# Kernel optimization log

Measured on AMD Instinct MI355X. Metric: run time of the kernel, lower is better.

The kernel has to match this reference:

```python
import jax, jax.numpy as jnp
import numpy as np

B, C_IN, C_OUT, C_KEY, N = 8, 512, 512, 256, 2048


def setup_inputs() -> dict:
    key = jax.random.key(0)
    k1, k2, k3, k4 = jax.random.split(key, 4)
    x = jax.random.normal(k1, (B, C_IN, N), dtype=jnp.float32)
    # Conv1d(kernel=1, bias=False) weights -> plain linear maps over channel dim
    Wq = jax.random.normal(k2, (C_KEY, C_IN), dtype=jnp.float32) * (1.0 / np.sqrt(C_IN))
    Wk = jax.random.normal(k3, (C_KEY, C_IN), dtype=jnp.float32) * (1.0 / np.sqrt(C_IN))
    Wv = jax.random.normal(k4, (C_OUT, C_IN), dtype=jnp.float32) * (1.0 / np.sqrt(C_IN))
    return {"x": x, "Wq": Wq, "Wk": Wk, "Wv": Wv}


def reference(x, Wq, Wk, Wv):
    # 1x1 conv projections: [B, C, N] -> [B, Ck/Co, N]
    q = jnp.einsum("oc,bcn->bon", Wq, x)
    k = jnp.einsum("oc,bcn->bon", Wk, x)
    v = jnpqv = jnp.einsum("oc,bcn->bon", Wv, x)
    # sim_map[b,i,j] = sum_c k[b,c,i] * q[b,c,j]  (unscaled)
    sim = jnp.einsum("bci,bcj->bij", k, q)  # [B, N, N]
    attn = jax.nn.softmax(sim, axis=-1)
    # out = value @ sim_map, then permute(0,2,1) -> [B, N, C_out]
    out = jnp.einsum("bck,bkm->bmc", jnpqv, attn)
    return out
```

## Files before the change

kernel.cpp:

```cpp
#include <hip/hip_runtime.h>

typedef _Float16 half8 __attribute__((ext_vector_type(8)));
typedef _Float16 half4v __attribute__((ext_vector_type(4)));
typedef _Float16 half2v __attribute__((ext_vector_type(2)));
typedef float f32x4 __attribute__((ext_vector_type(4)));

#define ASYNC_CP16(gp, lp)                                       \
  __builtin_amdgcn_global_load_lds(                              \
      (const __attribute__((address_space(1))) void*)(gp),       \
      (__attribute__((address_space(3))) void*)(lp), 16, 0, 0)

__global__ __launch_bounds__(256) void conv_w(const float* __restrict__ Wq,
                                              const float* __restrict__ Wk,
                                              const float* __restrict__ Wv,
                                              _Float16* __restrict__ Wb) {
  int idx = blockIdx.x * 256 + threadIdx.x;
  int row = idx >> 9;
  float v;
  if (row < 256)      v = Wq[idx];
  else if (row < 512) v = Wk[idx - 256 * 512];
  else                v = Wv[idx - 512 * 512];
  Wb[idx] = (_Float16)v;
}

__global__ __launch_bounds__(256) void conv_xT(const float* __restrict__ x,
                                               _Float16* __restrict__ xT) {
  __shared__ float T[32][33];
  const int b = blockIdx.z;
  const int n0 = blockIdx.x * 32, c0 = blockIdx.y * 32;
  const int t = threadIdx.x;
  const float* xb = x + (size_t)b * 512 * 2048;
  const int n2 = t & 15, cr = t >> 4;
#pragma unroll
  for (int r = 0; r < 2; r++) {
    int c = cr + r * 16;
    float2 v = *(const float2*)&xb[(size_t)(c0 + c) * 2048 + n0 + n2 * 2];
    T[c][n2 * 2] = v.x;
    T[c][n2 * 2 + 1] = v.y;
  }
  __syncthreads();
  _Float16* xtb = xT + (size_t)b * 2048 * 512;
  const int c2 = t & 15, nr = t >> 4;
#pragma unroll
  for (int r = 0; r < 2; r++) {
    int n = nr + r * 16;
    half2v h;
    h[0] = (_Float16)T[c2 * 2][n];
    h[1] = (_Float16)T[c2 * 2 + 1][n];
    *(half2v*)&xtb[(size_t)(n0 + n) * 512 + c0 + c2 * 2] = h;
  }
}

template <typename OutT, bool TR, bool STATS, bool PROJ3>
__global__ __launch_bounds__(256) void gemm_nt(
    const _Float16* __restrict__ A, const _Float16* __restrict__ B,
    OutT* __restrict__ C, OutT* __restrict__ C2, int K, int lda, int ldb,
    int ldc, int ldc2, long sA, long sB, long sC, float* __restrict__ pm,
    float* __restrict__ ps) {
  A += (size_t)blockIdx.z * sA;
  B += (size_t)blockIdx.z * sB;
  C += (size_t)blockIdx.z * sC;
  if constexpr (PROJ3) C2 += (size_t)blockIdx.z * sC;
  const int m_blk = blockIdx.y * 128, n_blk = blockIdx.x * 128;

  __shared__ _Float16 As[3][4096];
  __shared__ _Float16 Bs[3][4096];

  const int t = threadIdx.x;
  const int lane = t & 63, wave = t >> 6;
  const int quad = lane >> 4, l16 = lane & 15;
  const int wm = (wave & 1) * 64, wn = (wave >> 1) * 64;

  const int srow = 16 * wave + (lane >> 2);
  const int schunk = (lane & 3) ^ ((lane >> 3) & 3);
  const _Float16* gA0 = A + (size_t)(m_blk + srow) * lda + schunk * 8;
  const _Float16* gA1 = gA0 + (size_t)64 * lda;
  const _Float16* gB0 = B + (size_t)(n_blk + srow) * ldb + schunk * 8;
  const _Float16* gB1 = gB0 + (size_t)64 * ldb;
  const int lofs = wave * 512 + lane * 8;

  const int rchunk = (quad ^ ((l16 >> 1) & 3)) * 8;

  f32x4 acc[4][4] = {};

  ASYNC_CP16(gA0, &As[0][lofs]);
  ASYNC_CP16(gA1, &As[0][lofs + 2048]);
  ASYNC_CP16(gB0, &Bs[0][lofs]);
  ASYNC_CP16(gB1, &Bs[0][lofs + 2048]);
  if (32 < K) {
    ASYNC_CP16(gA0 + 32, &As[1][lofs]);
    ASYNC_CP16(gA1 + 32, &As[1][lofs + 2048]);
    ASYNC_CP16(gB0 + 32, &Bs[1][lofs]);
    ASYNC_CP16(gB1 + 32, &Bs[1][lofs + 2048]);
  }

  int ib = 0;
  for (int k0 = 0; k0 < K; k0 += 32) {
    if (k0 + 32 < K) {
      asm volatile("s_waitcnt vmcnt(4)\n\ts_barrier" ::: "memory");
    } else {
      asm volatile("s_waitcnt vmcnt(0)\n\ts_barrier" ::: "memory");
    }
    if (k0 + 64 < K) {
      int nb = ib + 2;
      if (nb >= 3) nb -= 3;
      ASYNC_CP16(gA0 + k0 + 64, &As[nb][lofs]);
      ASYNC_CP16(gA1 + k0 + 64, &As[nb][lofs + 2048]);
      ASYNC_CP16(gB0 + k0 + 64, &Bs[nb][lofs]);
      ASYNC_CP16(gB1 + k0 + 64, &Bs[nb][lofs + 2048]);
    }
    half8 af[4], bf[4];
#pragma unroll
    for (int i = 0; i < 4; i++) {
      af[i] = *(const half8*)&As[ib][(wm + i * 16 + l16) * 32 + rchunk];
      bf[i] = *(const half8*)&Bs[ib][(wn + i * 16 + l16) * 32 + rchunk];
    }
#pragma unroll
    for (int i = 0; i < 4; i++)
#pragma unroll
      for (int j = 0; j < 4; j++)
        acc[i][j] =
            __builtin_amdgcn_mfma_f32_16x16x32_f16(af[i], bf[j], acc[i][j], 0, 0, 0);
    ib++;
    if (ib == 3) ib = 0;
  }

#pragma unroll
  for (int i = 0; i < 4; i++) {
    const int m0 = m_blk + wm + i * 16 + quad * 4;
#pragma unroll
    for (int j = 0; j < 4; j++) {
      const int n0 = n_blk + wn + j * 16 + l16;
      if constexpr (PROJ3) {
        if (m_blk < 512) {
          half4v h;
#pragma unroll
          for (int r = 0; r < 4; r++) h[r] = (_Float16)acc[i][j][r];
          *(half4v*)&C[(size_t)n0 * ldc + m0] = h;
        } else {
#pragma unroll
          for (int r = 0; r < 4; r++)
            C2[(size_t)(m0 - 512 + r) * ldc2 + n0] = (OutT)acc[i][j][r];
        }
      } else if constexpr (TR) {
        if constexpr (sizeof(OutT) == 4) {
          *(f32x4*)&C[(size_t)n0 * ldc + m0] = acc[i][j];
        } else {
          half4v h;
#pragma unroll
          for (int r = 0; r < 4; r++) h[r] = (_Float16)acc[i][j][r];
          if constexpr (STATS) {
#pragma unroll
            for (int r = 0; r < 4; r++) acc[i][j][r] = (float)h[r];
          }
          *(half4v*)&C[(size_t)n0 * ldc + m0] = h;
        }
      } else {
#pragma unroll
        for (int r = 0; r < 4; r++)
          C[(size_t)(m0 + r) * ldc + n0] = (OutT)acc[i][j][r];
      }
    }
  }

  if constexpr (STATS) {
    __shared__ float sred[2][128][2];
    const int wng = wave >> 1;
    float bmax[4][4], bsum[4][4];
#pragma unroll
    for (int i = 0; i < 4; i++) {
#pragma unroll
      for (int r = 0; r < 4; r++) {
        float mx = acc[i][0][r];
#pragma unroll
        for (int j = 1; j < 4; j++) mx = fmaxf(mx, acc[i][j][r]);
#pragma unroll
        for (int d = 1; d < 16; d <<= 1)
          mx = fmaxf(mx, __shfl_xor(mx, d, 64));
        float es = 0.f;
#pragma unroll
        for (int j = 0; j < 4; j++) es += __expf(acc[i][j][r] - mx);
#pragma unroll
        for (int d = 1; d < 16; d <<= 1) es += __shfl_xor(es, d, 64);
        bmax[i][r] = mx;
        bsum[i][r] = es;
      }
    }
    if (l16 == 0) {
#pragma unroll
      for (int i = 0; i < 4; i++)
#pragma unroll
        for (int r = 0; r < 4; r++) {
          int ml = wm + i * 16 + quad * 4 + r;
          sred[wng][ml][0] = bmax[i][r];
          sred[wng][ml][1] = bsum[i][r];
        }
    }
    __syncthreads();
    if (t < 128) {
      float m0 = sred[0][t][0], s0 = sred[0][t][1];
      float m1 = sred[1][t][0], s1 = sred[1][t][1];
      float M = fmaxf(m0, m1);
      float S = s0 * __expf(m0 - M) + s1 * __expf(m1 - M);
      size_t o = ((size_t)blockIdx.z * 16 + blockIdx.x) * 2048 + m_blk + t;
      pm[o] = M;
      ps[o] = S;
    }
  }
}

__global__ __launch_bounds__(256) void colstats2(const float* __restrict__ pm,
                                                 const float* __restrict__ ps,
                                                 float* __restrict__ shift) {
  const int idx = blockIdx.x * 256 + threadIdx.x;
  const int b = idx >> 11, col = idx & 2047;
  const float* pmb = pm + (size_t)b * 16 * 2048 + col;
  const float* psb = ps + (size_t)b * 16 * 2048 + col;
  float m = -3.0e38f;
#pragma unroll
  for (int i = 0; i < 16; i++) m = fmaxf(m, pmb[(size_t)i * 2048]);
  float s = 0.f;
#pragma unroll
  for (int i = 0; i < 16; i++)
    s += psb[(size_t)i * 2048] * __expf(pmb[(size_t)i * 2048] - m);
  shift[idx] = m + __logf(s);
}

__global__ __launch_bounds__(256) void attnscale(_Float16* __restrict__ simH,
                                                 const float* __restrict__ shift) {
  const size_t b = blockIdx.y;
  const size_t g = (size_t)blockIdx.x * 256 + threadIdx.x;
  const int col = (int)(g & 255) * 8;
  _Float16* p = simH + b * (2048ull * 2048) + g * 8;
  half8 h = *(const half8*)p;
  f32x4 s0 = *(const f32x4*)(shift + b * 2048 + col);
  f32x4 s1 = *(const f32x4*)(shift + b * 2048 + col + 4);
  half8 o;
#pragma unroll
  for (int i = 0; i < 4; i++) {
    o[i] = (_Float16)__expf((float)h[i] - s0[i]);
    o[i + 4] = (_Float16)__expf((float)h[i + 4] - s1[i]);
  }
  *(half8*)p = o;
}

extern "C" void kernel_launch(void* const* d_in, const int* in_sizes, int n_in,
                              void* d_out, int out_size, void* d_ws,
                              size_t ws_size, hipStream_t stream) {
  const float* x = (const float*)d_in[0];
  const float* Wq = (const float*)d_in[1];
  const float* Wk = (const float*)d_in[2];
  const float* Wv = (const float*)d_in[3];
  float* out = (float*)d_out;

  char* p = (char*)d_ws;
  auto alloc = [&](size_t bytes) -> char* {
    char* r = p;
    p += (bytes + 255) & ~(size_t)255;
    return r;
  };
  const size_t NB = 8, N = 2048, CIN = 512, CO = 512;
  _Float16* Wb = (_Float16*)alloc(1024 * 512 * sizeof(_Float16));
  _Float16* xT = (_Float16*)alloc(NB * N * CIN * sizeof(_Float16));
  _Float16* qkT = (_Float16*)alloc(NB * N * 512 * sizeof(_Float16));
  _Float16* v = (_Float16*)alloc(NB * CO * N * sizeof(_Float16));
  size_t base_used = (size_t)(p - (char*)d_ws);

  const size_t per_b =
      (size_t)N * N * 2 + 2 * 16 * N * 4 + N * 4 + 8192;
  int cb = 8;
  while (cb > 1 && base_used + (size_t)cb * per_b > ws_size) cb >>= 1;
  _Float16* simH = (_Float16*)alloc((size_t)cb * N * N * 2);
  float* pm = (float*)alloc((size_t)cb * 16 * N * 4);
  float* ps = (float*)alloc((size_t)cb * 16 * N * 4);
  float* shift = (float*)alloc((size_t)cb * N * 4);

  conv_w<<<dim3(1024 * 512 / 256), 256, 0, stream>>>(Wq, Wk, Wv, Wb);
  conv_xT<<<dim3(64, 16, 8), 256, 0, stream>>>(x, xT);

  gemm_nt<_Float16, true, false, true><<<dim3(16, 8, 8), 256, 0, stream>>>(
      Wb, xT, qkT, v, 512, 512, 512, 512, 2048, 0, (long)(N * CIN),
      (long)(N * 512), nullptr, nullptr);

  for (int b0 = 0; b0 < 8; b0 += cb) {
    const _Float16* kT = qkT + (size_t)b0 * N * 512 + 256;
    const _Float16* qT = qkT + (size_t)b0 * N * 512;
    gemm_nt<_Float16, true, true, false><<<dim3(16, 16, cb), 256, 0, stream>>>(
        kT, qT, simH, nullptr, 256, 512, 512, 2048, 0, (long)(N * 512),
        (long)(N * 512), (long)(N * N), pm, ps);
    colstats2<<<dim3(cb * 8), 256, 0, stream>>>(pm, ps, shift);
    attnscale<<<dim3(2048, cb), 256, 0, stream>>>(simH, shift);
    gemm_nt<float, false, false, false><<<dim3(4, 16, cb), 256, 0, stream>>>(
        simH, v + (size_t)b0 * CO * N, out + (size_t)b0 * N * CO, nullptr,
        2048, 2048, 2048, 512, 0, (long)(N * N), (long)(CO * N),
        (long)(N * CO), nullptr, nullptr);
  }
}
```

Baseline: 239.2 us.

## Swap sim GEMM operands for non-transposed stores and use double buffering

The similarity GEMM now computes q^T k with A=q and B=k, so each output tile is stored in plain row-major order instead of through a transposed half4 store. The per-block max/sum statistics are reorganised to reduce across the M dimension (rows held within a lane and across quads) instead of using 16-lane shuffles. The sim kernel also switches from a triple-buffered to a double-buffered LDS pipeline, which lowers LDS use and may raise occupancy at the cost of less load latency hiding. The scalar row-major fp16 stores write 2 bytes per lane with consecutive lanes on consecutive columns; whether that beats the old 8-byte transposed stores is uncertain.

```diff
diff --git a/kernel.cpp b/kernel.cpp
--- a/kernel.cpp
+++ b/kernel.cpp
@@ -51,7 +51,7 @@
   }
 }
 
-template <typename OutT, bool TR, bool STATS, bool PROJ3>
+template <typename OutT, int BUFS, int MODE>
 __global__ __launch_bounds__(256) void gemm_nt(
     const _Float16* __restrict__ A, const _Float16* __restrict__ B,
     OutT* __restrict__ C, OutT* __restrict__ C2, int K, int lda, int ldb,
@@ -60,11 +60,11 @@
   A += (size_t)blockIdx.z * sA;
   B += (size_t)blockIdx.z * sB;
   C += (size_t)blockIdx.z * sC;
-  if constexpr (PROJ3) C2 += (size_t)blockIdx.z * sC;
+  if constexpr (MODE == 1) C2 += (size_t)blockIdx.z * sC;
   const int m_blk = blockIdx.y * 128, n_blk = blockIdx.x * 128;
 
-  __shared__ _Float16 As[3][4096];
-  __shared__ _Float16 Bs[3][4096];
+  __shared__ _Float16 As[BUFS][4096];
+  __shared__ _Float16 Bs[BUFS][4096];
 
   const int t = threadIdx.x;
   const int lane = t & 63, wave = t >> 6;
@@ -83,31 +83,34 @@
 
   f32x4 acc[4][4] = {};
 
-  ASYNC_CP16(gA0, &As[0][lofs]);
-  ASYNC_CP16(gA1, &As[0][lofs + 2048]);
-  ASYNC_CP16(gB0, &Bs[0][lofs]);
-  ASYNC_CP16(gB1, &Bs[0][lofs + 2048]);
-  if (32 < K) {
-    ASYNC_CP16(gA0 + 32, &As[1][lofs]);
-    ASYNC_CP16(gA1 + 32, &As[1][lofs + 2048]);
-    ASYNC_CP16(gB0 + 32, &Bs[1][lofs]);
-    ASYNC_CP16(gB1 + 32, &Bs[1][lofs + 2048]);
+#pragma unroll
+  for (int pb = 0; pb < BUFS - 1; pb++) {
+    if (pb * 32 < K) {
+      ASYNC_CP16(gA0 + pb * 32, &As[pb][lofs]);
+      ASYNC_CP16(gA1 + pb * 32, &As[pb][lofs + 2048]);
+      ASYNC_CP16(gB0 + pb * 32, &Bs[pb][lofs]);
+      ASYNC_CP16(gB1 + pb * 32, &Bs[pb][lofs + 2048]);
+    }
   }
 
   int ib = 0;
   for (int k0 = 0; k0 < K; k0 += 32) {
-    if (k0 + 32 < K) {
-      asm volatile("s_waitcnt vmcnt(4)\n\ts_barrier" ::: "memory");
+    if constexpr (BUFS == 3) {
+      if (k0 + 32 < K)
+        asm volatile("s_waitcnt vmcnt(4)\n\ts_barrier" ::: "memory");
+      else
+        asm volatile("s_waitcnt vmcnt(0)\n\ts_barrier" ::: "memory");
     } else {
       asm volatile("s_waitcnt vmcnt(0)\n\ts_barrier" ::: "memory");
     }
-    if (k0 + 64 < K) {
-      int nb = ib + 2;
-      if (nb >= 3) nb -= 3;
-      ASYNC_CP16(gA0 + k0 + 64, &As[nb][lofs]);
-      ASYNC_CP16(gA1 + k0 + 64, &As[nb][lofs + 2048]);
-      ASYNC_CP16(gB0 + k0 + 64, &Bs[nb][lofs]);
-      ASYNC_CP16(gB1 + k0 + 64, &Bs[nb][lofs + 2048]);
+    if (k0 + (BUFS - 1) * 32 < K) {
+      int nb = ib + BUFS - 1;
+      if (nb >= BUFS) nb -= BUFS;
+      const int ko = k0 + (BUFS - 1) * 32;
+      ASYNC_CP16(gA0 + ko, &As[nb][lofs]);
+      ASYNC_CP16(gA1 + ko, &As[nb][lofs + 2048]);
+      ASYNC_CP16(gB0 + ko, &Bs[nb][lofs]);
+      ASYNC_CP16(gB1 + ko, &Bs[nb][lofs + 2048]);
     }
     half8 af[4], bf[4];
 #pragma unroll
@@ -122,7 +125,7 @@
         acc[i][j] =
             __builtin_amdgcn_mfma_f32_16x16x32_f16(af[i], bf[j], acc[i][j], 0, 0, 0);
     ib++;
-    if (ib == 3) ib = 0;
+    if (ib == BUFS) ib = 0;
   }
 
 #pragma unroll
@@ -131,7 +134,7 @@
 #pragma unroll
     for (int j = 0; j < 4; j++) {
       const int n0 = n_blk + wn + j * 16 + l16;
-      if constexpr (PROJ3) {
+      if constexpr (MODE == 1) {
         if (m_blk < 512) {
           half4v h;
 #pragma unroll
@@ -142,18 +145,12 @@
           for (int r = 0; r < 4; r++)
             C2[(size_t)(m0 - 512 + r) * ldc2 + n0] = (OutT)acc[i][j][r];
         }
-      } else if constexpr (TR) {
-        if constexpr (sizeof(OutT) == 4) {
-          *(f32x4*)&C[(size_t)n0 * ldc + m0] = acc[i][j];
-        } else {
-          half4v h;
-#pragma unroll
-          for (int r = 0; r < 4; r++) h[r] = (_Float16)acc[i][j][r];
-          if constexpr (STATS) {
-#pragma unroll
-            for (int r = 0; r < 4; r++) acc[i][j][r] = (float)h[r];
-          }
-          *(half4v*)&C[(size_t)n0 * ldc + m0] = h;
+      } else if constexpr (MODE == 2) {
+#pragma unroll
+        for (int r = 0; r < 4; r++) {
+          _Float16 h = (_Float16)acc[i][j][r];
+          C[(size_t)(m0 + r) * ldc + n0] = h;
+          acc[i][j][r] = (float)h;
         }
       } else {
 #pragma unroll
@@ -163,46 +160,42 @@
     }
   }
 
-  if constexpr (STATS) {
-    __shared__ float sred[2][128][2];
-    const int wng = wave >> 1;
-    float bmax[4][4], bsum[4][4];
-#pragma unroll
-    for (int i = 0; i < 4; i++) {
-#pragma unroll
-      for (int r = 0; r < 4; r++) {
-        float mx = acc[i][0][r];
-#pragma unroll
-        for (int j = 1; j < 4; j++) mx = fmaxf(mx, acc[i][j][r]);
-#pragma unroll
-        for (int d = 1; d < 16; d <<= 1)
-          mx = fmaxf(mx, __shfl_xor(mx, d, 64));
-        float es = 0.f;
-#pragma unroll
-        for (int j = 0; j < 4; j++) es += __expf(acc[i][j][r] - mx);
-#pragma unroll
-        for (int d = 1; d < 16; d <<= 1) es += __shfl_xor(es, d, 64);
-        bmax[i][r] = mx;
-        bsum[i][r] = es;
+  if constexpr (MODE == 2) {
+    __shared__ float sred[128][2][2];
+    float pM[4], pS[4];
+#pragma unroll
+    for (int j = 0; j < 4; j++) {
+      float mx = acc[0][j][0];
+#pragma unroll
+      for (int i = 0; i < 4; i++)
+#pragma unroll
+        for (int r = 0; r < 4; r++) mx = fmaxf(mx, acc[i][j][r]);
+      mx = fmaxf(mx, __shfl_xor(mx, 16, 64));
+      mx = fmaxf(mx, __shfl_xor(mx, 32, 64));
+      float es = 0.f;
+#pragma unroll
+      for (int i = 0; i < 4; i++)
+#pragma unroll
+        for (int r = 0; r < 4; r++) es += __expf(acc[i][j][r] - mx);
+      es += __shfl_xor(es, 16, 64);
+      es += __shfl_xor(es, 32, 64);
+      pM[j] = mx;
+      pS[j] = es;
+    }
+    if (quad == 0) {
+#pragma unroll
+      for (int j = 0; j < 4; j++) {
+        sred[wn + j * 16 + l16][wave & 1][0] = pM[j];
+        sred[wn + j * 16 + l16][wave & 1][1] = pS[j];
       }
-    }
-    if (l16 == 0) {
-#pragma unroll
-      for (int i = 0; i < 4; i++)
-#pragma unroll
-        for (int r = 0; r < 4; r++) {
-          int ml = wm + i * 16 + quad * 4 + r;
-          sred[wng][ml][0] = bmax[i][r];
-          sred[wng][ml][1] = bsum[i][r];
-        }
     }
     __syncthreads();
     if (t < 128) {
-      float m0 = sred[0][t][0], s0 = sred[0][t][1];
-      float m1 = sred[1][t][0], s1 = sred[1][t][1];
+      float m0 = sred[t][0][0], s0 = sred[t][0][1];
+      float m1 = sred[t][1][0], s1 = sred[t][1][1];
       float M = fmaxf(m0, m1);
       float S = s0 * __expf(m0 - M) + s1 * __expf(m1 - M);
-      size_t o = ((size_t)blockIdx.z * 16 + blockIdx.x) * 2048 + m_blk + t;
+      size_t o = ((size_t)blockIdx.z * 16 + blockIdx.y) * 2048 + n_blk + t;
       pm[o] = M;
       ps[o] = S;
     }
@@ -278,19 +271,19 @@
   conv_w<<<dim3(1024 * 512 / 256), 256, 0, stream>>>(Wq, Wk, Wv, Wb);
   conv_xT<<<dim3(64, 16, 8), 256, 0, stream>>>(x, xT);
 
-  gemm_nt<_Float16, true, false, true><<<dim3(16, 8, 8), 256, 0, stream>>>(
+  gemm_nt<_Float16, 3, 1><<<dim3(16, 8, 8), 256, 0, stream>>>(
       Wb, xT, qkT, v, 512, 512, 512, 512, 2048, 0, (long)(N * CIN),
       (long)(N * 512), nullptr, nullptr);
 
   for (int b0 = 0; b0 < 8; b0 += cb) {
+    const _Float16* qT = qkT + (size_t)b0 * N * 512;
     const _Float16* kT = qkT + (size_t)b0 * N * 512 + 256;
-    const _Float16* qT = qkT + (size_t)b0 * N * 512;
-    gemm_nt<_Float16, true, true, false><<<dim3(16, 16, cb), 256, 0, stream>>>(
-        kT, qT, simH, nullptr, 256, 512, 512, 2048, 0, (long)(N * 512),
+    gemm_nt<_Float16, 2, 2><<<dim3(16, 16, cb), 256, 0, stream>>>(
+        qT, kT, simH, nullptr, 256, 512, 512, 2048, 0, (long)(N * 512),
         (long)(N * 512), (long)(N * N), pm, ps);
     colstats2<<<dim3(cb * 8), 256, 0, stream>>>(pm, ps, shift);
     attnscale<<<dim3(2048, cb), 256, 0, stream>>>(simH, shift);
-    gemm_nt<float, false, false, false><<<dim3(4, 16, cb), 256, 0, stream>>>(
+    gemm_nt<float, 3, 0><<<dim3(4, 16, cb), 256, 0, stream>>>(
         simH, v + (size_t)b0 * CO * N, out + (size_t)b0 * N * CO, nullptr,
         2048, 2048, 2048, 512, 0, (long)(N * N), (long)(CO * N),
         (long)(N * CO), nullptr, nullptr);
```

Result: faster. 229.3 us (-4.2%).
